# Kernel tuning notes

Measured on AMD Instinct MI355X. Metric: run time of the kernel, lower is better.

Reference implementation:

```python
import jax, jax.numpy as jnp
import numpy as np

GAMMA = 0.001

N_TEST, N_TRAIN, D, OUT = 8192, 8192, 512, 16

def setup_inputs() -> dict:
    key = jax.random.key(0)
    k1, k2, k3 = jax.random.split(key, 3)
    X = jax.random.normal(k1, (N_TEST, D), dtype=jnp.float32)
    train_X = jax.random.normal(k2, (N_TRAIN, D), dtype=jnp.float32)
    alpha = jax.random.normal(k3, (N_TRAIN, OUT), dtype=jnp.float32)
    return {"X": X, "train_X": train_X, "alpha": alpha}


def reference(X, train_X, alpha):
    # (same math as (x[:,None]-y[None])**2 summed over d, without the n*m*d blowup)
    x_sq = jnp.sum(X * X, axis=-1, keepdims=True)            # [n_test, 1]
    y_sq = jnp.sum(train_X * train_X, axis=-1)[None, :]       # [1, n_train]
    cross = X @ train_X.T                                     # [n_test, n_train]
    sq = x_sq + y_sq - 2.0 * cross
    K_test = jnp.exp(-GAMMA * sq)
    return K_test @ alpha                                     # [n_test, out]
```

## Files before the change

### kernel.cpp

```cpp
#include <hip/hip_runtime.h>
#include <stdint.h>

#define NROW 8192
#define DIM  512
#define NOUT 16
#define GAMMA 0.001f
#define EXP2S (2.0f * GAMMA * 1.44269504088896340736f)

typedef __bf16 bf16_t;
typedef bf16_t bf16x4_t __attribute__((ext_vector_type(4)));
typedef bf16_t bf16x8_t __attribute__((ext_vector_type(8)));
typedef float  floatx4_t __attribute__((ext_vector_type(4)));
typedef long   longx2_t __attribute__((ext_vector_type(2)));

__device__ __forceinline__ void async_copy16(const void* g, const void* l) {
    __builtin_amdgcn_global_load_lds(
        (__attribute__((address_space(1))) void*)(uintptr_t)g,
        (__attribute__((address_space(3))) void*)(uint32_t)(uintptr_t)l,
        16, 0, 0);
}

__global__ __launch_bounds__(256) void prep_convert(
    const float* __restrict__ X, const float* __restrict__ T,
    const float* __restrict__ alpha,
    uint8_t* __restrict__ Xf, uint8_t* __restrict__ Tf,
    float* __restrict__ xfac, bf16_t* __restrict__ alphaTp)
{
    const int w = threadIdx.x >> 6, lane = threadIdx.x & 63;
    const int row = blockIdx.x * 4 + w;
    const bool is_test = row < NROW;
    const float* src = is_test ? X : T;
    uint8_t* dst = is_test ? Xf : Tf;
    const int r = is_test ? row : row - NROW;
    const float4* s4 = (const float4*)(src + (size_t)r * DIM);
    const float4 v0 = s4[lane * 2];
    const float4 v1 = s4[lane * 2 + 1];
    float ss = v0.x*v0.x + v0.y*v0.y + v0.z*v0.z + v0.w*v0.w
             + v1.x*v1.x + v1.y*v1.y + v1.z*v1.z + v1.w*v1.w;
    int lo = __builtin_amdgcn_cvt_pk_fp8_f32(v0.x, v0.y, 0, false);
    lo     = __builtin_amdgcn_cvt_pk_fp8_f32(v0.z, v0.w, lo, true);
    int hi = __builtin_amdgcn_cvt_pk_fp8_f32(v1.x, v1.y, 0, false);
    hi     = __builtin_amdgcn_cvt_pk_fp8_f32(v1.z, v1.w, hi, true);
    const int off = (lane >> 3) * 64 + (lane & 3) * 16 + ((lane >> 2) & 1) * 8;
    *(int2*)(dst + (size_t)r * DIM + off) = make_int2(lo, hi);
#pragma unroll
    for (int m = 32; m > 0; m >>= 1) ss += __shfl_xor(ss, m, 64);
    const float f = __expf(-GAMMA * ss);
    if (is_test) {
        if (lane == 0) xfac[r] = f;
    } else if (lane < 16) {
        alphaTp[(size_t)lane * NROW + r] = (bf16_t)(alpha[r * 16 + lane] * f);
    }
}

#define TPT 4
#define KLD2 72

__global__ __launch_bounds__(256, 3) void rbf_main(
    const uint8_t* __restrict__ Xf, const uint8_t* __restrict__ Tf,
    const bf16_t* __restrict__ alphaTp, const float* __restrict__ xfac,
    float* __restrict__ out)
{
    __shared__ __align__(16) unsigned char smem[4 * 64 * KLD2 * 2];

    const int tid = threadIdx.x;
    const int w = tid >> 6, lane = tid & 63;
    const int wm = w >> 1, wn = w & 1;
    const int quad = lane >> 4, l15 = lane & 15;

    const int rb = blockIdx.x;
    const int chunk = blockIdx.y;
    const int row0 = rb * 128;
    const int cb0 = chunk * (TPT * 128);

    const int s_row = tid >> 2;
    const int g_off = (((tid & 3) ^ ((s_row >> 1) & 3)) * 16);
    const uint8_t* gX = Xf + (size_t)(row0 + s_row) * DIM + g_off;
    const uint8_t* gT = Tf + (size_t)(cb0 + s_row) * DIM + g_off;
    const unsigned ldsW = (unsigned)(w << 10);

    const int xs = ((quad ^ ((l15 >> 1) & 3)) * 16);

    const floatx4_t vzero = {0.f, 0.f, 0.f, 0.f};
    floatx4_t oacc[4];
#pragma unroll
    for (int i = 0; i < 4; ++i) oacc[i] = vzero;

    bf16_t* kw = (bf16_t*)smem + w * (64 * KLD2);

    for (int t = 0; t < TPT; ++t) {
        const int cb = cb0 + t * 128;
        const uint8_t* gTt = gT + (size_t)t * 128 * DIM;

        floatx4_t acc[4][4];
#pragma unroll
        for (int i = 0; i < 4; ++i)
#pragma unroll
            for (int j = 0; j < 4; ++j) acc[i][j] = vzero;

        __syncthreads();
#pragma unroll
        for (int i = 0; i < 2; ++i) {
            async_copy16(gTt + (size_t)i * 64 * DIM, smem + i * 4096 + ldsW);
            async_copy16(gX  + (size_t)i * 64 * DIM, smem + 8192 + i * 4096 + ldsW);
        }

#pragma unroll
        for (int g = 0; g < 8; ++g) {
            __syncthreads();
            if (g < 7) {
                unsigned bn = ((g + 1) & 1) * 16384u;
                const int kb = (g + 1) * 64;
#pragma unroll
                for (int i = 0; i < 2; ++i) {
                    async_copy16(gTt + (size_t)i * 64 * DIM + kb, smem + bn + i * 4096 + ldsW);
                    async_copy16(gX  + (size_t)i * 64 * DIM + kb, smem + bn + 8192 + i * 4096 + ldsW);
                }
            }
            const unsigned char* bufc = smem + (g & 1) * 16384;
            longx2_t ta[4], xb[4];
#pragma unroll
            for (int i = 0; i < 4; ++i) {
                ta[i] = *(const longx2_t*)(bufc + (wm * 64 + i * 16 + l15) * 64 + xs);
                xb[i] = *(const longx2_t*)(bufc + 8192 + (wn * 64 + i * 16 + l15) * 64 + xs);
            }
#pragma unroll
            for (int mi = 0; mi < 4; ++mi)
#pragma unroll
                for (int ni = 0; ni < 4; ++ni)
                    acc[mi][ni] = __builtin_amdgcn_mfma_f32_16x16x32_fp8_fp8(
                        ta[mi].x, xb[ni].x, acc[mi][ni], 0, 0, 0);
#pragma unroll
            for (int mi = 0; mi < 4; ++mi)
#pragma unroll
                for (int ni = 0; ni < 4; ++ni)
                    acc[mi][ni] = __builtin_amdgcn_mfma_f32_16x16x32_fp8_fp8(
                        ta[mi].y, xb[ni].y, acc[mi][ni], 0, 0, 0);
        }

        __syncthreads();
#pragma unroll
        for (int ni = 0; ni < 4; ++ni)
#pragma unroll
            for (int mi = 0; mi < 4; ++mi) {
                bf16x4_t pk;
#pragma unroll
                for (int r = 0; r < 4; ++r)
                    pk[r] = (bf16_t)__builtin_amdgcn_exp2f(acc[mi][ni][r] * EXP2S);
                *(bf16x4_t*)(kw + (ni * 16 + l15) * KLD2 + mi * 16 + quad * 4) = pk;
            }

#pragma unroll
        for (int ks = 0; ks < 2; ++ks) {
            const bf16x8_t bv = *(const bf16x8_t*)(alphaTp + (size_t)l15 * NROW
                                                   + cb + wm * 64 + ks * 32 + quad * 8);
#pragma unroll
            for (int ni = 0; ni < 4; ++ni) {
                const bf16x8_t av = *(const bf16x8_t*)(kw + (ni * 16 + l15) * KLD2
                                                       + ks * 32 + quad * 8);
                oacc[ni] = __builtin_amdgcn_mfma_f32_16x16x32_bf16(av, bv, oacc[ni], 0, 0, 0);
            }
        }
    }

    __syncthreads();
    float* stash = (float*)smem;
    if (wm == 1) {
#pragma unroll
        for (int ni = 0; ni < 4; ++ni)
            *(floatx4_t*)(stash + wn * 1024 + ni * 256 + lane * 4) = oacc[ni];
    }
    __syncthreads();
    if (wm == 0) {
#pragma unroll
        for (int ni = 0; ni < 4; ++ni) {
            const floatx4_t o2 = *(const floatx4_t*)(stash + wn * 1024 + ni * 256 + lane * 4);
            const int trow = row0 + wn * 64 + ni * 16 + quad * 4;
            const float4 xf = *(const float4*)(xfac + trow);
            atomicAdd(out + (size_t)(trow + 0) * NOUT + l15, (oacc[ni][0] + o2[0]) * xf.x);
            atomicAdd(out + (size_t)(trow + 1) * NOUT + l15, (oacc[ni][1] + o2[1]) * xf.y);
            atomicAdd(out + (size_t)(trow + 2) * NOUT + l15, (oacc[ni][2] + o2[2]) * xf.z);
            atomicAdd(out + (size_t)(trow + 3) * NOUT + l15, (oacc[ni][3] + o2[3]) * xf.w);
        }
    }
}

extern "C" void kernel_launch(void* const* d_in, const int* in_sizes, int n_in,
                              void* d_out, int out_size, void* d_ws, size_t ws_size,
                              hipStream_t stream) {
    (void)in_sizes; (void)n_in; (void)out_size; (void)ws_size;
    const float* X     = (const float*)d_in[0];
    const float* T     = (const float*)d_in[1];
    const float* alpha = (const float*)d_in[2];

    char* ws = (char*)d_ws;
    uint8_t* Xf     = (uint8_t*)ws;
    uint8_t* Tf     = (uint8_t*)(ws + (8u << 20));
    float*   xfac   = (float*)(ws + (16u << 20));
    bf16_t*  alphaTp= (bf16_t*)(ws + (16u << 20) + (64u << 10));
    float*   out    = (float*)d_out;

    hipMemsetAsync(out, 0, (size_t)NROW * NOUT * sizeof(float), stream);
    prep_convert<<<4096, 256, 0, stream>>>(X, T, alpha, Xf, Tf, xfac, alphaTp);
    dim3 grid(64, 16);
    rbf_main<<<grid, 256, 0, stream>>>(Xf, Tf, alphaTp, xfac, out);
}
```

Measured before the change: 129.3 us.

## Keep the X tile resident in registers across all train tiles

Loads the block's 128-row test tile once at kernel start into 128 registers per thread (xr[8][4] longx2) and reuses it for every train tile, instead of re-streaming X through LDS on each of the TPT iterations. This halves the per-iteration global-to-LDS traffic and LDS reads, and shrinks the double buffer. In exchange, register pressure rises sharply, so the launch bound drops from 3 to 2 blocks per CU, lowering occupancy and the latency hiding that comes with it.

```diff
diff --git a/kernel.cpp b/kernel.cpp
--- a/kernel.cpp
+++ b/kernel.cpp
@@ -56,7 +56,7 @@
 #define TPT 4
 #define KLD2 72
 
-__global__ __launch_bounds__(256, 3) void rbf_main(
+__global__ __launch_bounds__(256, 2) void rbf_main(
     const uint8_t* __restrict__ Xf, const uint8_t* __restrict__ Tf,
     const bf16_t* __restrict__ alphaTp, const float* __restrict__ xfac,
     float* __restrict__ out)
@@ -81,6 +81,26 @@
 
     const int xs = ((quad ^ ((l15 >> 1) & 3)) * 16);
 
+    longx2_t xr[8][4];
+#pragma unroll
+    for (int i = 0; i < 2; ++i)
+        async_copy16(gX + (size_t)i * 64 * DIM, smem + i * 4096 + ldsW);
+#pragma unroll
+    for (int g = 0; g < 8; ++g) {
+        __syncthreads();
+        if (g < 7) {
+            const unsigned bn = ((g + 1) & 1) * 8192u;
+#pragma unroll
+            for (int i = 0; i < 2; ++i)
+                async_copy16(gX + (size_t)i * 64 * DIM + (g + 1) * 64,
+                             smem + bn + i * 4096 + ldsW);
+        }
+        const unsigned char* bufc = smem + (g & 1) * 8192;
+#pragma unroll
+        for (int i = 0; i < 4; ++i)
+            xr[g][i] = *(const longx2_t*)(bufc + (wn * 64 + i * 16 + l15) * 64 + xs);
+    }
+
     const floatx4_t vzero = {0.f, 0.f, 0.f, 0.f};
     floatx4_t oacc[4];
 #pragma unroll
@@ -100,42 +120,37 @@
 
         __syncthreads();
 #pragma unroll
-        for (int i = 0; i < 2; ++i) {
+        for (int i = 0; i < 2; ++i)
             async_copy16(gTt + (size_t)i * 64 * DIM, smem + i * 4096 + ldsW);
-            async_copy16(gX  + (size_t)i * 64 * DIM, smem + 8192 + i * 4096 + ldsW);
-        }
 
 #pragma unroll
         for (int g = 0; g < 8; ++g) {
             __syncthreads();
             if (g < 7) {
-                unsigned bn = ((g + 1) & 1) * 16384u;
+                const unsigned bn = ((g + 1) & 1) * 8192u;
                 const int kb = (g + 1) * 64;
 #pragma unroll
-                for (int i = 0; i < 2; ++i) {
-                    async_copy16(gTt + (size_t)i * 64 * DIM + kb, smem + bn + i * 4096 + ldsW);
-                    async_copy16(gX  + (size_t)i * 64 * DIM + kb, smem + bn + 8192 + i * 4096 + ldsW);
-                }
+                for (int i = 0; i < 2; ++i)
+                    async_copy16(gTt + (size_t)i * 64 * DIM + kb,
+                                 smem + bn + i * 4096 + ldsW);
             }
-            const unsigned char* bufc = smem + (g & 1) * 16384;
-            longx2_t ta[4], xb[4];
-#pragma unroll
-            for (int i = 0; i < 4; ++i) {
+            const unsigned char* bufc = smem + (g & 1) * 8192;
+            longx2_t ta[4];
+#pragma unroll
+            for (int i = 0; i < 4; ++i)
                 ta[i] = *(const longx2_t*)(bufc + (wm * 64 + i * 16 + l15) * 64 + xs);
-                xb[i] = *(const longx2_t*)(bufc + 8192 + (wn * 64 + i * 16 + l15) * 64 + xs);
-            }
 #pragma unroll
             for (int mi = 0; mi < 4; ++mi)
 #pragma unroll
                 for (int ni = 0; ni < 4; ++ni)
                     acc[mi][ni] = __builtin_amdgcn_mfma_f32_16x16x32_fp8_fp8(
-                        ta[mi].x, xb[ni].x, acc[mi][ni], 0, 0, 0);
+                        ta[mi].x, xr[g][ni].x, acc[mi][ni], 0, 0, 0);
 #pragma unroll
             for (int mi = 0; mi < 4; ++mi)
 #pragma unroll
                 for (int ni = 0; ni < 4; ++ni)
                     acc[mi][ni] = __builtin_amdgcn_mfma_f32_16x16x32_fp8_fp8(
-                        ta[mi].y, xb[ni].y, acc[mi][ni], 0, 0, 0);
+                        ta[mi].y, xr[g][ni].y, acc[mi][ni], 0, 0, 0);
         }
 
         __syncthreads();
```

After: 130.4 us. About the same (+0.9%).

## Use gfx950 scaled 16x16x128 fp8 MFMA with 128-byte K tiles

Applied to the files above, without the earlier changes.

Replaces the pair of 16x16x32 fp8 MFMAs per K-step with the CDNA4 scaled 16x16x128 f8f6f4 MFMA, using unit scale exponents (0x7F). The K tile grows from 64 to 128 bytes per stage, halving the pipeline stages. The LDS layout changes to 128-byte rows with an 8-way XOR swizzle, and prep writes fp8 rows linearly instead of pre-permuted. LDS grows to 64KB and launch bounds drop to 2 blocks per SM, trading occupancy for higher MFMA throughput and fewer barriers.

```diff
diff --git a/kernel.cpp b/kernel.cpp
--- a/kernel.cpp
+++ b/kernel.cpp
@@ -6,12 +6,14 @@
 #define NOUT 16
 #define GAMMA 0.001f
 #define EXP2S (2.0f * GAMMA * 1.44269504088896340736f)
+#define SC1 0x7F7F7F7F
 
 typedef __bf16 bf16_t;
 typedef bf16_t bf16x4_t __attribute__((ext_vector_type(4)));
 typedef bf16_t bf16x8_t __attribute__((ext_vector_type(8)));
 typedef float  floatx4_t __attribute__((ext_vector_type(4)));
-typedef long   longx2_t __attribute__((ext_vector_type(2)));
+typedef int    intx4_t  __attribute__((ext_vector_type(4)));
+typedef int    intx8_t  __attribute__((ext_vector_type(8)));
 
 __device__ __forceinline__ void async_copy16(const void* g, const void* l) {
     __builtin_amdgcn_global_load_lds(
@@ -41,8 +43,7 @@
     lo     = __builtin_amdgcn_cvt_pk_fp8_f32(v0.z, v0.w, lo, true);
     int hi = __builtin_amdgcn_cvt_pk_fp8_f32(v1.x, v1.y, 0, false);
     hi     = __builtin_amdgcn_cvt_pk_fp8_f32(v1.z, v1.w, hi, true);
-    const int off = (lane >> 3) * 64 + (lane & 3) * 16 + ((lane >> 2) & 1) * 8;
-    *(int2*)(dst + (size_t)r * DIM + off) = make_int2(lo, hi);
+    *(int2*)(dst + (size_t)r * DIM + lane * 8) = make_int2(lo, hi);
 #pragma unroll
     for (int m = 32; m > 0; m >>= 1) ss += __shfl_xor(ss, m, 64);
     const float f = __expf(-GAMMA * ss);
@@ -56,12 +57,12 @@
 #define TPT 4
 #define KLD2 72
 
-__global__ __launch_bounds__(256, 3) void rbf_main(
+__global__ __launch_bounds__(256, 2) void rbf_main(
     const uint8_t* __restrict__ Xf, const uint8_t* __restrict__ Tf,
     const bf16_t* __restrict__ alphaTp, const float* __restrict__ xfac,
     float* __restrict__ out)
 {
-    __shared__ __align__(16) unsigned char smem[4 * 64 * KLD2 * 2];
+    __shared__ __align__(16) unsigned char smem[65536];
 
     const int tid = threadIdx.x;
     const int w = tid >> 6, lane = tid & 63;
@@ -73,13 +74,13 @@
     const int row0 = rb * 128;
     const int cb0 = chunk * (TPT * 128);
 
-    const int s_row = tid >> 2;
-    const int g_off = (((tid & 3) ^ ((s_row >> 1) & 3)) * 16);
-    const uint8_t* gX = Xf + (size_t)(row0 + s_row) * DIM + g_off;
-    const uint8_t* gT = Tf + (size_t)(cb0 + s_row) * DIM + g_off;
+    const int s_row = tid >> 3;
+    const int s_ub = (((tid & 7) ^ (s_row & 7)) * 16);
+    const uint8_t* gXp = Xf + (size_t)(row0 + s_row) * DIM + s_ub;
+    const uint8_t* gTp = Tf + (size_t)(cb0 + s_row) * DIM + s_ub;
     const unsigned ldsW = (unsigned)(w << 10);
 
-    const int xs = ((quad ^ ((l15 >> 1) & 3)) * 16);
+    const int sw = l15 & 7;
 
     const floatx4_t vzero = {0.f, 0.f, 0.f, 0.f};
     floatx4_t oacc[4];
@@ -90,7 +91,7 @@
 
     for (int t = 0; t < TPT; ++t) {
         const int cb = cb0 + t * 128;
-        const uint8_t* gTt = gT + (size_t)t * 128 * DIM;
+        const uint8_t* gTt = gTp + (size_t)t * 128 * DIM;
 
         floatx4_t acc[4][4];
 #pragma unroll
@@ -100,42 +101,42 @@
 
         __syncthreads();
 #pragma unroll
-        for (int i = 0; i < 2; ++i) {
-            async_copy16(gTt + (size_t)i * 64 * DIM, smem + i * 4096 + ldsW);
-            async_copy16(gX  + (size_t)i * 64 * DIM, smem + 8192 + i * 4096 + ldsW);
-        }
-
-#pragma unroll
-        for (int g = 0; g < 8; ++g) {
+        for (int i = 0; i < 4; ++i) {
+            async_copy16(gTt + (size_t)i * 16384, smem + i * 4096 + ldsW);
+            async_copy16(gXp + (size_t)i * 16384, smem + 16384 + i * 4096 + ldsW);
+        }
+
+#pragma unroll
+        for (int g = 0; g < 4; ++g) {
             __syncthreads();
-            if (g < 7) {
-                unsigned bn = ((g + 1) & 1) * 16384u;
-                const int kb = (g + 1) * 64;
-#pragma unroll
-                for (int i = 0; i < 2; ++i) {
-                    async_copy16(gTt + (size_t)i * 64 * DIM + kb, smem + bn + i * 4096 + ldsW);
-                    async_copy16(gX  + (size_t)i * 64 * DIM + kb, smem + bn + 8192 + i * 4096 + ldsW);
+            if (g < 3) {
+                const unsigned bb = ((g + 1) & 1) * 32768u;
+                const int kb = (g + 1) * 128;
+#pragma unroll
+                for (int i = 0; i < 4; ++i) {
+                    async_copy16(gTt + (size_t)i * 16384 + kb, smem + bb + i * 4096 + ldsW);
+                    async_copy16(gXp + (size_t)i * 16384 + kb, smem + bb + 16384 + i * 4096 + ldsW);
                 }
             }
-            const unsigned char* bufc = smem + (g & 1) * 16384;
-            longx2_t ta[4], xb[4];
+            const unsigned char* bufc = smem + (g & 1) * 32768;
+            intx8_t ta[4], xb[4];
 #pragma unroll
             for (int i = 0; i < 4; ++i) {
-                ta[i] = *(const longx2_t*)(bufc + (wm * 64 + i * 16 + l15) * 64 + xs);
-                xb[i] = *(const longx2_t*)(bufc + 8192 + (wn * 64 + i * 16 + l15) * 64 + xs);
+                const int rA = wm * 64 + i * 16 + l15;
+                const intx4_t alo = *(const intx4_t*)(bufc + rA * 128 + (((2 * quad) ^ sw) * 16));
+                const intx4_t ahi = *(const intx4_t*)(bufc + rA * 128 + (((2 * quad + 1) ^ sw) * 16));
+                ta[i] = __builtin_shufflevector(alo, ahi, 0, 1, 2, 3, 4, 5, 6, 7);
+                const int rB = wn * 64 + i * 16 + l15;
+                const intx4_t blo = *(const intx4_t*)(bufc + 16384 + rB * 128 + (((2 * quad) ^ sw) * 16));
+                const intx4_t bhi = *(const intx4_t*)(bufc + 16384 + rB * 128 + (((2 * quad + 1) ^ sw) * 16));
+                xb[i] = __builtin_shufflevector(blo, bhi, 0, 1, 2, 3, 4, 5, 6, 7);
             }
 #pragma unroll
             for (int mi = 0; mi < 4; ++mi)
 #pragma unroll
                 for (int ni = 0; ni < 4; ++ni)
-                    acc[mi][ni] = __builtin_amdgcn_mfma_f32_16x16x32_fp8_fp8(
-                        ta[mi].x, xb[ni].x, acc[mi][ni], 0, 0, 0);
-#pragma unroll
-            for (int mi = 0; mi < 4; ++mi)
-#pragma unroll
-                for (int ni = 0; ni < 4; ++ni)
-                    acc[mi][ni] = __builtin_amdgcn_mfma_f32_16x16x32_fp8_fp8(
-                        ta[mi].y, xb[ni].y, acc[mi][ni], 0, 0, 0);
+                    acc[mi][ni] = __builtin_amdgcn_mfma_scale_f32_16x16x128_f8f6f4(
+                        ta[mi], xb[ni], acc[mi][ni], 0, 0, 0, SC1, 0, SC1);
         }
 
         __syncthreads();
```

New measurement: 121.3 us. 6.2% less time.
